# Kernel tuning notes

Hardware: AMD Instinct MI355X
Metric: run time of the kernel (lower is better)

The kernel has to match this reference:

```python
import jax, jax.numpy as jnp
import numpy as np
import math


def _rel_pos_tables(W):
    # continuous relative coords table: [(2W-1), (2W-1), 2]
    c = np.arange(-(W - 1), W, dtype=np.float32)
    table = np.stack(np.meshgrid(c, c, indexing='ij'), axis=-1)  # [2W-1,2W-1,2]
    table = table / (W - 1)
    table = table * 8.0
    table = np.sign(table) * np.log2(np.abs(table) + 1.0) / math.log2(8.0)
    # relative position index: [W*W, W*W]
    coords = np.stack(np.meshgrid(np.arange(W), np.arange(W), indexing='ij'))  # [2,W,W]
    flat = coords.reshape(2, -1)  # [2, W*W]
    rel = flat[:, :, None] - flat[:, None, :]  # [2, N, N]
    rel = rel.transpose(1, 2, 0).copy()
    rel[:, :, 0] += W - 1
    rel[:, :, 1] += W - 1
    rel[:, :, 0] *= 2 * W - 1
    idx = rel.sum(-1)  # [N, N]
    return jnp.asarray(table), jnp.asarray(idx, dtype=jnp.int32)


def setup_inputs() -> dict:
    key = jax.random.key(0)
    ks = jax.random.split(key, 10)
    dim, W, H = 512, 8, 16
    N = W * W
    B_, nW = 2048, 256
    s = 0.02
    inp = {
        'x': jax.random.normal(ks[0], (B_, N, dim), jnp.float32),
        'mask': jax.random.normal(ks[1], (nW, N, N), jnp.float32),
        'qkv_w': jax.random.normal(ks[2], (dim, 3 * dim), jnp.float32) * s,
        'qkv_b': jnp.zeros((3 * dim,), jnp.float32),
        'logit_scale': jnp.full((H, 1, 1), math.log(10.0), jnp.float32),
        'cpb_w1': jax.random.normal(ks[3], (2, 512), jnp.float32) * s,
        'cpb_b1': jnp.zeros((512,), jnp.float32),
        'cpb_w2': jax.random.normal(ks[4], (512, H), jnp.float32) * s,
        'proj_w': jax.random.normal(ks[5], (dim, dim), jnp.float32) * s,
        'proj_b': jnp.zeros((dim,), jnp.float32),
        'window_size': W,
        'num_heads': H,
    }
    return inp


def reference(x, mask, qkv_w, qkv_b, logit_scale, cpb_w1, cpb_b1, cpb_w2,
              proj_w, proj_b, window_size, num_heads):
    B_, N, C = x.shape
    H = num_heads
    hd = C // H

    qkv = (x @ qkv_w + qkv_b).reshape(B_, N, 3, H, hd)
    qkv = jnp.transpose(qkv, (2, 0, 3, 1, 4))  # [3, B_, H, N, hd]
    q, k, v = qkv[0], qkv[1], qkv[2]

    # cosine attention: L2-normalize q, k (eps matches F.normalize)
    q = q / jnp.clip(jnp.linalg.norm(q, axis=-1, keepdims=True), 1e-12)
    k = k / jnp.clip(jnp.linalg.norm(k, axis=-1, keepdims=True), 1e-12)

    attn = jnp.einsum('bhnd,bhmd->bhnm', q, k)
    scale = jnp.exp(jnp.minimum(logit_scale, math.log(1.0 / 0.01)))  # [H,1,1]
    attn = attn * scale[None]

    # continuous relative position bias
    table, idx = _rel_pos_tables(window_size)
    t = jax.nn.relu(table @ cpb_w1 + cpb_b1) @ cpb_w2  # [2W-1, 2W-1, H]
    t = t.reshape(-1, H)
    bias = t[idx.reshape(-1)].reshape(N, N, H)
    bias = 16.0 * jax.nn.sigmoid(jnp.transpose(bias, (2, 0, 1)))  # [H, N, N]
    attn = attn + bias[None]

    # mask add: [nW, N, N]
    nW = mask.shape[0]
    attn = attn.reshape(B_ // nW, nW, H, N, N) + mask[None, :, None]
    attn = attn.reshape(B_, H, N, N)

    attn = jax.nn.softmax(attn, axis=-1)
    out = jnp.einsum('bhnm,bhmd->bhnd', attn, v)
    out = jnp.transpose(out, (0, 2, 1, 3)).reshape(B_, N, C)
    out = out @ proj_w + proj_b
    return out
```

## Files before the change

kernel.cpp:

```cpp
#include <hip/hip_runtime.h>
#include <hip/hip_bf16.h>
#include <stdint.h>

typedef __attribute__((ext_vector_type(8))) short short8;
typedef __attribute__((ext_vector_type(8))) _Float16 half8;
typedef __attribute__((ext_vector_type(4))) float f32x4;

__device__ __forceinline__ unsigned short f2h(float f) {
  union { _Float16 h; unsigned short u; } c;
  c.h = (_Float16)f;
  return c.u;
}
__device__ __forceinline__ float h2f(unsigned short u) {
  union { _Float16 h; unsigned short u; } c;
  c.u = u;
  return (float)c.h;
}
__device__ __forceinline__ void gload_lds16(const void* g, void* l) {
  __builtin_amdgcn_global_load_lds(
      (const __attribute__((address_space(1))) unsigned int*)g,
      (__attribute__((address_space(3))) unsigned int*)l, 16, 0, 0);
}


__global__ __launch_bounds__(256) void cast_f16(const float* __restrict__ in,
                                                unsigned short* __restrict__ out) {
  const size_t total = (size_t)131072 * 512 / 8;
  size_t stride = (size_t)gridDim.x * 256;
  for (size_t i = blockIdx.x * 256 + threadIdx.x; i < total; i += stride) {
    f32x4 f0 = *(const f32x4*)(in + i * 8);
    f32x4 f1 = *(const f32x4*)(in + i * 8 + 4);
    short8 o;
#pragma unroll
    for (int e = 0; e < 4; e++) {
      o[e] = (short)f2h(f0[e]);
      o[4 + e] = (short)f2h(f1[e]);
    }
    *(short8*)(out + i * 8) = o;
  }
}

__global__ __launch_bounds__(256) void transpose_cast(const float* __restrict__ in,
                                                      unsigned short* __restrict__ out,
                                                      int K, int N) {
  __shared__ float tile[32][33];
  int nb = N / 32;
  int bx = blockIdx.x % nb, by = blockIdx.x / nb;
  int tx = threadIdx.x & 31, ty = threadIdx.x >> 5;
#pragma unroll
  for (int r = 0; r < 32; r += 8)
    tile[ty + r][tx] = in[(size_t)(by * 32 + ty + r) * N + bx * 32 + tx];
  __syncthreads();
#pragma unroll
  for (int r = 0; r < 32; r += 8)
    out[(size_t)(bx * 32 + ty + r) * K + by * 32 + tx] = f2h(tile[tx][ty + r]);
}

__device__ __forceinline__ float cpb_coord(int a) {
  float v = (float)(a - 7) * (8.0f / 7.0f);
  float s = (v > 0.f) ? 1.f : ((v < 0.f) ? -1.f : 0.f);
  return s * log2f(fabsf(v) + 1.f) * (1.f / 3.f);
}

__global__ __launch_bounds__(64) void cpb_mlp(const float* __restrict__ w1,
                                              const float* __restrict__ b1,
                                              const float* __restrict__ w2,
                                              float* __restrict__ t_out) {
  int e = blockIdx.x;
  int dy = e / 15, dx = e % 15;
  float in0 = cpb_coord(dy), in1 = cpb_coord(dx);
  float acc[16];
#pragma unroll
  for (int o = 0; o < 16; ++o) acc[o] = 0.f;
  for (int u = threadIdx.x; u < 512; u += 64) {
    float hsum = fmaxf(in0 * w1[u] + in1 * w1[512 + u] + b1[u], 0.f);
#pragma unroll
    for (int o = 0; o < 16; ++o) acc[o] += hsum * w2[u * 16 + o];
  }
#pragma unroll
  for (int o = 0; o < 16; ++o) {
    float v = acc[o];
    v += __shfl_xor(v, 1);  v += __shfl_xor(v, 2);  v += __shfl_xor(v, 4);
    v += __shfl_xor(v, 8);  v += __shfl_xor(v, 16); v += __shfl_xor(v, 32);
    acc[o] = v;
  }
  if (threadIdx.x == 0)
#pragma unroll
    for (int o = 0; o < 16; ++o) t_out[e * 16 + o] = acc[o];
}

__global__ __launch_bounds__(256) void bias_kernel(const float* __restrict__ t,
                                                   float* __restrict__ bias) {
  int idx = blockIdx.x * 256 + threadIdx.x;
  int j = idx & 63, i = (idx >> 6) & 63, h = idx >> 12;
  int dy = (i >> 3) - (j >> 3) + 7;
  int dx = (i & 7) - (j & 7) + 7;
  float v = t[(dy * 15 + dx) * 16 + h];
  bias[idx] = 16.f / (1.f + expf(-v));
}

__global__ __launch_bounds__(512, 2) void qkv_gemm(const unsigned short* __restrict__ xh,
                                                   const unsigned short* __restrict__ Wt,
                                                   const float* __restrict__ bvec,
                                                   unsigned short* __restrict__ qout,
                                                   unsigned short* __restrict__ kout,
                                                   unsigned short* __restrict__ vout) {
  __shared__ __align__(16) short smem[65536];
  const int bid = (blockIdx.x & 7) * 384 + (blockIdx.x >> 3);
  const int nt = bid % 6;
  const int mt = bid / 6;
  const int m0 = mt * 256, n0 = nt * 256;
  const int t = threadIdx.x;
  const int l = t & 63, wid = t >> 6;
  const int wm = wid >> 2, wn = wid & 3;
  const int fr = l & 15, fg = l >> 4;

  f32x4 acc[8][4];
#pragma unroll
  for (int i = 0; i < 8; i++)
#pragma unroll
    for (int j = 0; j < 4; j++) acc[i][j] = f32x4{0.f, 0.f, 0.f, 0.f};

  auto STAGE = [&](int bsel, int kt) {
#pragma unroll
    for (int it = 0; it < 4; ++it) {
      int flat = it * 512 + t;
      int row = flat >> 3, c = flat & 7;
      gload_lds16(xh + (size_t)(m0 + row) * 512 + kt * 64 + c * 8,
                  &smem[bsel * 16384 + row * 64 + c * 8]);
      gload_lds16(Wt + (size_t)(n0 + row) * 512 + kt * 64 + c * 8,
                  &smem[32768 + bsel * 16384 + row * 64 + c * 8]);
    }
  };

  STAGE(0, 0);
  __builtin_amdgcn_sched_barrier(0);
  asm volatile("s_waitcnt vmcnt(0)" ::: "memory");
  __builtin_amdgcn_sched_barrier(0);
  __builtin_amdgcn_s_barrier();
  __builtin_amdgcn_sched_barrier(0);

  int cur = 0;
  for (int kt = 0; kt < 8; ++kt) {
    if (kt < 7) STAGE(cur ^ 1, kt + 1);
    __builtin_amdgcn_sched_barrier(0);
    {
      const short* Ab = &smem[cur * 16384];
      const short* Bb = &smem[32768 + cur * 16384];
      half8 bfr[4][2];
#pragma unroll
      for (int j = 0; j < 4; ++j)
#pragma unroll
        for (int kk = 0; kk < 2; ++kk)
          bfr[j][kk] = *(const half8*)&Bb[(wn * 64 + j * 16 + fr) * 64 + kk * 32 + fg * 8];
#pragma unroll
      for (int i = 0; i < 8; ++i) {
        half8 a0 = *(const half8*)&Ab[(wm * 128 + i * 16 + fr) * 64 + fg * 8];
        half8 a1 = *(const half8*)&Ab[(wm * 128 + i * 16 + fr) * 64 + 32 + fg * 8];
#pragma unroll
        for (int j = 0; j < 4; ++j) {
          acc[i][j] = __builtin_amdgcn_mfma_f32_16x16x32_f16(a0, bfr[j][0], acc[i][j], 0, 0, 0);
          acc[i][j] = __builtin_amdgcn_mfma_f32_16x16x32_f16(a1, bfr[j][1], acc[i][j], 0, 0, 0);
        }
      }
    }
    __builtin_amdgcn_sched_barrier(0);
    asm volatile("s_waitcnt vmcnt(0)" ::: "memory");
    __builtin_amdgcn_sched_barrier(0);
    __builtin_amdgcn_s_barrier();
    __builtin_amdgcn_sched_barrier(0);
    cur ^= 1;
  }

  unsigned short* dst;
  int coloff;
  if (nt < 2)      { dst = qout; coloff = nt * 256; }
  else if (nt < 4) { dst = kout; coloff = (nt - 2) * 256; }
  else             { dst = vout; coloff = (nt - 4) * 256; }
#pragma unroll
  for (int hh = 0; hh < 2; ++hh) {
    if (hh) __syncthreads();
    if (wm == hh) {
#pragma unroll
      for (int i = 0; i < 8; ++i)
#pragma unroll
        for (int j = 0; j < 4; ++j) {
          int col = wn * 64 + j * 16 + fr;
          float bb = bvec[n0 + col];
#pragma unroll
          for (int r = 0; r < 4; ++r)
            smem[(i * 16 + fg * 4 + r) * 256 + col] = (short)f2h(acc[i][j][r] + bb);
        }
    }
    __syncthreads();
#pragma unroll
    for (int it = 0; it < 8; ++it) {
      int flat = it * 512 + t;
      int row = flat >> 5, c32 = flat & 31;
      *(short8*)(dst + (size_t)(m0 + hh * 128 + row) * 512 + coloff + c32 * 8) =
          *(short8*)&smem[row * 256 + c32 * 8];
    }
  }
}

__global__ __launch_bounds__(256) void attn_kernel(const unsigned short* __restrict__ qws,
                                                   const unsigned short* __restrict__ kws,
                                                   const unsigned short* __restrict__ vws,
                                                   const float* __restrict__ bias,
                                                   const float* __restrict__ mask,
                                                   const float* __restrict__ logit_scale,
                                                   unsigned short* __restrict__ aout) {
  const int blk = (blockIdx.x & 7) * 4096 + (blockIdx.x >> 3);
  const int h = blk & 15;
  const int b = blk >> 4;
  const int wmi = b & 255;
  const int t = threadIdx.x, l = t & 63, w = t >> 6;

  __shared__ __align__(16) short qs[64 * 32], ks[64 * 32];
  __shared__ __align__(16) short vt[32 * 72];
  __shared__ __align__(16) short plds[4 * 16 * 72];
  __shared__ float invs[64];

  const float scale = __expf(fminf(logit_scale[h], 4.6051702f));

  {
    const int r = t >> 2, c4 = t & 3;
    {
      uint4 raw = *(const uint4*)(qws + (size_t)(b * 64 + r) * 512 + h * 32 + c4 * 8);
      unsigned int rr[4] = {raw.x, raw.y, raw.z, raw.w};
      float f[8];
#pragma unroll
      for (int e = 0; e < 4; e++) {
        f[2 * e]     = h2f((unsigned short)(rr[e] & 0xffff));
        f[2 * e + 1] = h2f((unsigned short)(rr[e] >> 16));
      }
      float ss = 0.f;
#pragma unroll
      for (int e = 0; e < 8; e++) ss += f[e] * f[e];
      ss += __shfl_xor(ss, 1);
      ss += __shfl_xor(ss, 2);
      float inv = 1.f / fmaxf(sqrtf(ss), 1e-12f);
      short8 o;
#pragma unroll
      for (int e = 0; e < 8; e++) o[e] = (short)f2h(f[e] * inv);
      *(short8*)&qs[r * 32 + c4 * 8] = o;
    }
    {
      uint4 raw = *(const uint4*)(kws + (size_t)(b * 64 + r) * 512 + h * 32 + c4 * 8);
      unsigned int rr[4] = {raw.x, raw.y, raw.z, raw.w};
      float f[8];
#pragma unroll
      for (int e = 0; e < 4; e++) {
        f[2 * e]     = h2f((unsigned short)(rr[e] & 0xffff));
        f[2 * e + 1] = h2f((unsigned short)(rr[e] >> 16));
      }
      float ss = 0.f;
#pragma unroll
      for (int e = 0; e < 8; e++) ss += f[e] * f[e];
      ss += __shfl_xor(ss, 1);
      ss += __shfl_xor(ss, 2);
      float inv = 1.f / fmaxf(sqrtf(ss), 1e-12f);
      short8 o;
#pragma unroll
      for (int e = 0; e < 8; e++) o[e] = (short)f2h(f[e] * inv);
      *(short8*)&ks[r * 32 + c4 * 8] = o;
    }
    {
      uint4 raw = *(const uint4*)(vws + (size_t)(b * 64 + r) * 512 + h * 32 + c4 * 8);
      unsigned int rr[4] = {raw.x, raw.y, raw.z, raw.w};
#pragma unroll
      for (int e2 = 0; e2 < 4; e2++) {
        vt[(c4 * 8 + 2 * e2 + 0) * 72 + r] = (short)(rr[e2] & 0xffff);
        vt[(c4 * 8 + 2 * e2 + 1) * 72 + r] = (short)(rr[e2] >> 16);
      }
    }
  }
  __syncthreads();

  const int fr = l & 15, fg = l >> 4;
  half8 bq = *(half8*)&qs[(w * 16 + fr) * 32 + fg * 8];

  f32x4 st[4];
#pragma unroll
  for (int kt = 0; kt < 4; kt++) {
    half8 ak = *(half8*)&ks[(kt * 16 + fr) * 32 + fg * 8];
    st[kt] = __builtin_amdgcn_mfma_f32_16x16x32_f16(ak, bq, f32x4{0.f, 0.f, 0.f, 0.f}, 0, 0, 0);
  }
  const int q = w * 16 + fr;
  const int kbase = fg * 4;
  float sv[16];
  float mx = -1e30f;
#pragma unroll
  for (int kt = 0; kt < 4; kt++) {
    f32x4 b4 = *(const f32x4*)&bias[(size_t)(h * 64 + q) * 64 + kt * 16 + kbase];
    f32x4 m4 = *(const f32x4*)&mask[(size_t)(wmi * 64 + q) * 64 + kt * 16 + kbase];
#pragma unroll
    for (int j = 0; j < 4; j++) {
      float xv = st[kt][j] * scale + b4[j] + m4[j];
      sv[kt * 4 + j] = xv;
      mx = fmaxf(mx, xv);
    }
  }
  mx = fmaxf(mx, __shfl_xor(mx, 16));
  mx = fmaxf(mx, __shfl_xor(mx, 32));
  float sum = 0.f;
#pragma unroll
  for (int i2 = 0; i2 < 16; i2++) {
    float p = __expf(sv[i2] - mx);
    sv[i2] = p;
    sum += p;
  }
  sum += __shfl_xor(sum, 16);
  sum += __shfl_xor(sum, 32);

  short* pl = &plds[w * 16 * 72];
#pragma unroll
  for (int kt = 0; kt < 4; kt++)
#pragma unroll
    for (int j = 0; j < 4; j += 2) {
      unsigned int pack = (unsigned int)f2h(sv[kt * 4 + j]) |
                          ((unsigned int)f2h(sv[kt * 4 + j + 1]) << 16);
      *(unsigned int*)&pl[fr * 72 + kt * 16 + kbase + j] = pack;
    }
  if (fg == 0) invs[q] = 1.f / sum;
  __syncthreads();

  half8 pa0 = *(half8*)&pl[fr * 72 + fg * 8];
  half8 pa1 = *(half8*)&pl[fr * 72 + 32 + fg * 8];
#pragma unroll
  for (int nt2 = 0; nt2 < 2; nt2++) {
    half8 bv0 = *(half8*)&vt[(nt2 * 16 + fr) * 72 + fg * 8];
    half8 bv1 = *(half8*)&vt[(nt2 * 16 + fr) * 72 + 32 + fg * 8];
    f32x4 o = f32x4{0.f, 0.f, 0.f, 0.f};
    o = __builtin_amdgcn_mfma_f32_16x16x32_f16(pa0, bv0, o, 0, 0, 0);
    o = __builtin_amdgcn_mfma_f32_16x16x32_f16(pa1, bv1, o, 0, 0, 0);
    const int qo = w * 16 + fg * 4;
    const int hd = nt2 * 16 + fr;
#pragma unroll
    for (int r2 = 0; r2 < 4; r2++) {
      float vv = o[r2] * invs[qo + r2];
      qs[(qo + r2) * 32 + hd] = (short)f2h(vv);
    }
  }
  __syncthreads();
  {
    const int row = t >> 2, c = t & 3;
    *(short8*)(aout + (size_t)(b * 64 + row) * 512 + h * 32 + c * 8) =
        *(short8*)&qs[row * 32 + c * 8];
  }
}

__global__ __launch_bounds__(256) void proj_gemm(const unsigned short* __restrict__ A,
                                                 const unsigned short* __restrict__ Wt,
                                                 const float* __restrict__ bvec,
                                                 float* __restrict__ out) {
  __shared__ __align__(16) short smem[16384];
  const int bid = (blockIdx.x & 7) * 512 + (blockIdx.x >> 3);
  const int nt = bid & 3;
  const int mt = bid >> 2;
  const int m0 = mt * 128, n0 = nt * 128;
  const int t = threadIdx.x;
  const int l = t & 63, w = t >> 6;
  const int wm = w >> 1, wn = w & 1;
  const int fr = l & 15, fg = l >> 4;
  const int sch = t & 3;

  f32x4 acc[4][4];
#pragma unroll
  for (int i = 0; i < 4; i++)
#pragma unroll
    for (int j = 0; j < 4; j++) acc[i][j] = f32x4{0.f, 0.f, 0.f, 0.f};

  auto STAGE = [&](int bsel, int k0) {
#pragma unroll
    for (int it = 0; it < 2; ++it) {
      int flat = it * 256 + t;
      int row = flat >> 2;
      gload_lds16(A + (size_t)(m0 + row) * 512 + k0 + sch * 8,
                  &smem[bsel * 4096 + flat * 8]);
      gload_lds16(Wt + (size_t)(n0 + row) * 512 + k0 + sch * 8,
                  &smem[8192 + bsel * 4096 + flat * 8]);
    }
  };

  STAGE(0, 0);
  __syncthreads();
  int cur = 0;
  for (int k0 = 0; k0 < 512; k0 += 32) {
    if (k0 + 32 < 512) STAGE(cur ^ 1, k0 + 32);
    half8 af[4], bfr[4];
#pragma unroll
    for (int i = 0; i < 4; i++)
      af[i] = *(half8*)&smem[cur * 4096 + (wm * 64 + i * 16 + fr) * 32 + fg * 8];
#pragma unroll
    for (int j = 0; j < 4; j++)
      bfr[j] = *(half8*)&smem[8192 + cur * 4096 + (wn * 64 + j * 16 + fr) * 32 + fg * 8];
#pragma unroll
    for (int i = 0; i < 4; i++)
#pragma unroll
      for (int j = 0; j < 4; j++)
        acc[i][j] = __builtin_amdgcn_mfma_f32_16x16x32_f16(af[i], bfr[j], acc[i][j], 0, 0, 0);
    __syncthreads();
    cur ^= 1;
  }

  float* bounce = (float*)smem;
#pragma unroll
  for (int half = 0; half < 2; ++half) {
    if (wm == half) {
#pragma unroll
      for (int j = 0; j < 4; j++) {
        int col = wn * 64 + j * 16 + fr;
        float bb = bvec[n0 + col];
#pragma unroll
        for (int i = 0; i < 4; i++) {
          int row0 = i * 16 + fg * 4;
#pragma unroll
          for (int r = 0; r < 4; r++)
            bounce[(row0 + r) * 128 + col] = acc[i][j][r] + bb;
        }
      }
    }
    __syncthreads();
#pragma unroll
    for (int it = 0; it < 8; ++it) {
      int flat = it * 256 + t;
      int row = flat >> 5, c4 = flat & 31;
      *(f32x4*)(out + (size_t)(m0 + half * 64 + row) * 512 + n0 + c4 * 4) =
          *(f32x4*)&bounce[row * 128 + c4 * 4];
    }
    __syncthreads();
  }
}

extern "C" void kernel_launch(void* const* d_in, const int* in_sizes, int n_in,
                              void* d_out, int out_size, void* d_ws, size_t ws_size,
                              hipStream_t stream) {
  const float* x           = (const float*)d_in[0];
  const float* mask        = (const float*)d_in[1];
  const float* qkv_w       = (const float*)d_in[2];
  const float* qkv_b       = (const float*)d_in[3];
  const float* logit_scale = (const float*)d_in[4];
  const float* cpb_w1      = (const float*)d_in[5];
  const float* cpb_b1      = (const float*)d_in[6];
  const float* cpb_w2      = (const float*)d_in[7];
  const float* proj_w      = (const float*)d_in[8];
  const float* proj_b      = (const float*)d_in[9];
  (void)in_sizes; (void)n_in; (void)out_size; (void)ws_size;

  char* p = (char*)d_ws;
  unsigned short* Wqkv_t  = (unsigned short*)p; p += (size_t)1536 * 512 * 2;
  unsigned short* Wproj_t = (unsigned short*)p; p += (size_t)512 * 512 * 2;
  float* t_cpb            = (float*)p;          p += (size_t)225 * 16 * 4;
  float* biasb            = (float*)p;          p += (size_t)16 * 64 * 64 * 4;
  unsigned short* xh      = (unsigned short*)p; p += (size_t)131072 * 512 * 2;
  unsigned short* qbuf    = (unsigned short*)p; p += (size_t)131072 * 512 * 2;
  unsigned short* kbuf    = (unsigned short*)p; p += (size_t)131072 * 512 * 2;
  unsigned short* vbuf    = (unsigned short*)p; p += (size_t)131072 * 512 * 2;
  unsigned short* abuf    = (unsigned short*)p; p += (size_t)131072 * 512 * 2;

  cast_f16<<<2048, 256, 0, stream>>>(x, xh);
  transpose_cast<<<768, 256, 0, stream>>>(qkv_w, Wqkv_t, 512, 1536);
  transpose_cast<<<256, 256, 0, stream>>>(proj_w, Wproj_t, 512, 512);
  cpb_mlp<<<225, 64, 0, stream>>>(cpb_w1, cpb_b1, cpb_w2, t_cpb);
  bias_kernel<<<256, 256, 0, stream>>>(t_cpb, biasb);
  qkv_gemm<<<3072, 512, 0, stream>>>(xh, Wqkv_t, qkv_b, qbuf, kbuf, vbuf);
  attn_kernel<<<32768, 256, 0, stream>>>(qbuf, kbuf, vbuf, biasb, mask, logit_scale, abuf);
  proj_gemm<<<4096, 256, 0, stream>>>(abuf, Wproj_t, proj_b, (float*)d_out);
}
```

Baseline: 737.2 us.

## Fuse q/k L2 normalization into QKV GEMM epilogue and load q/k directly to LDS

Moves the per-head L2 normalization of q and k from the attention kernel into the QKV projection GEMM epilogue. There the fp32 accumulators are reduced across 16 lanes with shuffles and scaled before the fp16 store. The attention kernel then copies q and k straight from global memory into LDS with global_load_lds, skipping the convert/normalize/repack work. Normalizing before rounding to fp16 slightly changes numerics, and the GEMM epilogue gains shuffle and sqrt work.

```diff
diff --git a/kernel.cpp b/kernel.cpp
--- a/kernel.cpp
+++ b/kernel.cpp
@@ -172,6 +172,40 @@
     cur ^= 1;
   }
 
+#pragma unroll
+  for (int j = 0; j < 4; ++j) {
+    float bb = bvec[n0 + wn * 64 + j * 16 + fr];
+#pragma unroll
+    for (int i = 0; i < 8; ++i)
+#pragma unroll
+      for (int r = 0; r < 4; ++r) acc[i][j][r] += bb;
+  }
+
+  if (nt < 4) {
+#pragma unroll
+    for (int i = 0; i < 8; ++i) {
+#pragma unroll
+      for (int hh2 = 0; hh2 < 2; ++hh2) {
+        f32x4 ss;
+#pragma unroll
+        for (int r = 0; r < 4; ++r)
+          ss[r] = acc[i][2 * hh2][r] * acc[i][2 * hh2][r] +
+                  acc[i][2 * hh2 + 1][r] * acc[i][2 * hh2 + 1][r];
+#pragma unroll
+        for (int d = 1; d <= 8; d <<= 1) {
+#pragma unroll
+          for (int r = 0; r < 4; ++r) ss[r] += __shfl_xor(ss[r], d);
+        }
+#pragma unroll
+        for (int r = 0; r < 4; ++r) {
+          float inv = 1.f / fmaxf(sqrtf(ss[r]), 1e-12f);
+          acc[i][2 * hh2][r] *= inv;
+          acc[i][2 * hh2 + 1][r] *= inv;
+        }
+      }
+    }
+  }
+
   unsigned short* dst;
   int coloff;
   if (nt < 2)      { dst = qout; coloff = nt * 256; }
@@ -186,10 +220,9 @@
 #pragma unroll
         for (int j = 0; j < 4; ++j) {
           int col = wn * 64 + j * 16 + fr;
-          float bb = bvec[n0 + col];
 #pragma unroll
           for (int r = 0; r < 4; ++r)
-            smem[(i * 16 + fg * 4 + r) * 256 + col] = (short)f2h(acc[i][j][r] + bb);
+            smem[(i * 16 + fg * 4 + r) * 256 + col] = (short)f2h(acc[i][j][r]);
         }
     }
     __syncthreads();
@@ -225,54 +258,14 @@
 
   {
     const int r = t >> 2, c4 = t & 3;
-    {
-      uint4 raw = *(const uint4*)(qws + (size_t)(b * 64 + r) * 512 + h * 32 + c4 * 8);
-      unsigned int rr[4] = {raw.x, raw.y, raw.z, raw.w};
-      float f[8];
-#pragma unroll
-      for (int e = 0; e < 4; e++) {
-        f[2 * e]     = h2f((unsigned short)(rr[e] & 0xffff));
-        f[2 * e + 1] = h2f((unsigned short)(rr[e] >> 16));
-      }
-      float ss = 0.f;
-#pragma unroll
-      for (int e = 0; e < 8; e++) ss += f[e] * f[e];
-      ss += __shfl_xor(ss, 1);
-      ss += __shfl_xor(ss, 2);
-      float inv = 1.f / fmaxf(sqrtf(ss), 1e-12f);
-      short8 o;
-#pragma unroll
-      for (int e = 0; e < 8; e++) o[e] = (short)f2h(f[e] * inv);
-      *(short8*)&qs[r * 32 + c4 * 8] = o;
-    }
-    {
-      uint4 raw = *(const uint4*)(kws + (size_t)(b * 64 + r) * 512 + h * 32 + c4 * 8);
-      unsigned int rr[4] = {raw.x, raw.y, raw.z, raw.w};
-      float f[8];
-#pragma unroll
-      for (int e = 0; e < 4; e++) {
-        f[2 * e]     = h2f((unsigned short)(rr[e] & 0xffff));
-        f[2 * e + 1] = h2f((unsigned short)(rr[e] >> 16));
-      }
-      float ss = 0.f;
-#pragma unroll
-      for (int e = 0; e < 8; e++) ss += f[e] * f[e];
-      ss += __shfl_xor(ss, 1);
-      ss += __shfl_xor(ss, 2);
-      float inv = 1.f / fmaxf(sqrtf(ss), 1e-12f);
-      short8 o;
-#pragma unroll
-      for (int e = 0; e < 8; e++) o[e] = (short)f2h(f[e] * inv);
-      *(short8*)&ks[r * 32 + c4 * 8] = o;
-    }
-    {
-      uint4 raw = *(const uint4*)(vws + (size_t)(b * 64 + r) * 512 + h * 32 + c4 * 8);
-      unsigned int rr[4] = {raw.x, raw.y, raw.z, raw.w};
-#pragma unroll
-      for (int e2 = 0; e2 < 4; e2++) {
-        vt[(c4 * 8 + 2 * e2 + 0) * 72 + r] = (short)(rr[e2] & 0xffff);
-        vt[(c4 * 8 + 2 * e2 + 1) * 72 + r] = (short)(rr[e2] >> 16);
-      }
+    gload_lds16(qws + (size_t)(b * 64 + r) * 512 + h * 32 + c4 * 8, &qs[t * 8]);
+    gload_lds16(kws + (size_t)(b * 64 + r) * 512 + h * 32 + c4 * 8, &ks[t * 8]);
+    uint4 raw = *(const uint4*)(vws + (size_t)(b * 64 + r) * 512 + h * 32 + c4 * 8);
+    unsigned int rr[4] = {raw.x, raw.y, raw.z, raw.w};
+#pragma unroll
+    for (int e2 = 0; e2 < 4; e2++) {
+      vt[(c4 * 8 + 2 * e2 + 0) * 72 + r] = (short)(rr[e2] & 0xffff);
+      vt[(c4 * 8 + 2 * e2 + 1) * 72 + r] = (short)(rr[e2] >> 16);
     }
   }
   __syncthreads();
```

Result: slower. 822.9 us (+11.6%).

## Triple-buffer QKV GEMM with 32-wide K tiles and XOR-swizzled LDS

Applied to the files above, without the earlier changes.

The QKV GEMM main loop goes from double buffering with K=64 tiles to a three-stage ring of K=32 tiles. Prefetch now runs two tiles ahead, with partial vmcnt waits so loads overlap more MFMA work. LDS rows are XOR-swizzled to reduce bank conflicts on fragment reads. The shared buffer shrinks, but launch bounds drop to one block per CU, which may reduce occupancy, and each tile does less compute per barrier.

```diff
diff --git a/kernel.cpp b/kernel.cpp
--- a/kernel.cpp
+++ b/kernel.cpp
@@ -99,13 +99,13 @@
   bias[idx] = 16.f / (1.f + expf(-v));
 }
 
-__global__ __launch_bounds__(512, 2) void qkv_gemm(const unsigned short* __restrict__ xh,
+__global__ __launch_bounds__(512, 1) void qkv_gemm(const unsigned short* __restrict__ xh,
                                                    const unsigned short* __restrict__ Wt,
                                                    const float* __restrict__ bvec,
                                                    unsigned short* __restrict__ qout,
                                                    unsigned short* __restrict__ kout,
                                                    unsigned short* __restrict__ vout) {
-  __shared__ __align__(16) short smem[65536];
+  __shared__ __align__(16) short smem[49152];
   const int bid = (blockIdx.x & 7) * 384 + (blockIdx.x >> 3);
   const int nt = bid % 6;
   const int mt = bid / 6;
@@ -123,53 +123,52 @@
 
   auto STAGE = [&](int bsel, int kt) {
 #pragma unroll
-    for (int it = 0; it < 4; ++it) {
+    for (int it = 0; it < 2; ++it) {
       int flat = it * 512 + t;
-      int row = flat >> 3, c = flat & 7;
-      gload_lds16(xh + (size_t)(m0 + row) * 512 + kt * 64 + c * 8,
-                  &smem[bsel * 16384 + row * 64 + c * 8]);
-      gload_lds16(Wt + (size_t)(n0 + row) * 512 + kt * 64 + c * 8,
-                  &smem[32768 + bsel * 16384 + row * 64 + c * 8]);
+      int row = flat >> 2, s = flat & 3;
+      int g = s ^ (row & 3);
+      gload_lds16(xh + (size_t)(m0 + row) * 512 + kt * 32 + g * 8,
+                  &smem[bsel * 8192 + flat * 8]);
+      gload_lds16(Wt + (size_t)(n0 + row) * 512 + kt * 32 + g * 8,
+                  &smem[24576 + bsel * 8192 + flat * 8]);
     }
   };
 
   STAGE(0, 0);
+  STAGE(1, 1);
   __builtin_amdgcn_sched_barrier(0);
-  asm volatile("s_waitcnt vmcnt(0)" ::: "memory");
-  __builtin_amdgcn_sched_barrier(0);
-  __builtin_amdgcn_s_barrier();
-  __builtin_amdgcn_sched_barrier(0);
-
-  int cur = 0;
-  for (int kt = 0; kt < 8; ++kt) {
-    if (kt < 7) STAGE(cur ^ 1, kt + 1);
+
+  for (int kt = 0; kt < 16; ++kt) {
+    const int cur = kt % 3;
+    if (kt < 14) STAGE((kt + 2) % 3, kt + 2);
     __builtin_amdgcn_sched_barrier(0);
-    {
-      const short* Ab = &smem[cur * 16384];
-      const short* Bb = &smem[32768 + cur * 16384];
-      half8 bfr[4][2];
-#pragma unroll
-      for (int j = 0; j < 4; ++j)
-#pragma unroll
-        for (int kk = 0; kk < 2; ++kk)
-          bfr[j][kk] = *(const half8*)&Bb[(wn * 64 + j * 16 + fr) * 64 + kk * 32 + fg * 8];
-#pragma unroll
-      for (int i = 0; i < 8; ++i) {
-        half8 a0 = *(const half8*)&Ab[(wm * 128 + i * 16 + fr) * 64 + fg * 8];
-        half8 a1 = *(const half8*)&Ab[(wm * 128 + i * 16 + fr) * 64 + 32 + fg * 8];
-#pragma unroll
-        for (int j = 0; j < 4; ++j) {
-          acc[i][j] = __builtin_amdgcn_mfma_f32_16x16x32_f16(a0, bfr[j][0], acc[i][j], 0, 0, 0);
-          acc[i][j] = __builtin_amdgcn_mfma_f32_16x16x32_f16(a1, bfr[j][1], acc[i][j], 0, 0, 0);
-        }
-      }
-    }
-    __builtin_amdgcn_sched_barrier(0);
-    asm volatile("s_waitcnt vmcnt(0)" ::: "memory");
+    if (kt < 14)       asm volatile("s_waitcnt vmcnt(8)" ::: "memory");
+    else if (kt == 14) asm volatile("s_waitcnt vmcnt(4)" ::: "memory");
+    else               asm volatile("s_waitcnt vmcnt(0)" ::: "memory");
     __builtin_amdgcn_sched_barrier(0);
     __builtin_amdgcn_s_barrier();
     __builtin_amdgcn_sched_barrier(0);
-    cur ^= 1;
+    {
+      const short* Ab = &smem[cur * 8192];
+      const short* Bb = &smem[24576 + cur * 8192];
+      half8 bfr[4];
+#pragma unroll
+      for (int j = 0; j < 4; ++j) {
+        int row = wn * 64 + j * 16 + fr;
+        bfr[j] = *(const half8*)&Bb[row * 32 + ((fg ^ (row & 3)) << 3)];
+      }
+#pragma unroll
+      for (int i = 0; i < 8; ++i) {
+        int rowA = wm * 128 + i * 16 + fr;
+        half8 a0 = *(const half8*)&Ab[rowA * 32 + ((fg ^ (rowA & 3)) << 3)];
+#pragma unroll
+        for (int j = 0; j < 4; ++j)
+          acc[i][j] = __builtin_amdgcn_mfma_f32_16x16x32_f16(a0, bfr[j], acc[i][j], 0, 0, 0);
+      }
+    }
+    __builtin_amdgcn_sched_barrier(0);
+    __builtin_amdgcn_s_barrier();
+    __builtin_amdgcn_sched_barrier(0);
   }
 
   unsigned short* dst;
```

After: 732.0 us. About the same (-0.7%).
